# Kernel tuning notes

Measured on AMD Instinct MI355X. Metric: run time of the kernel, lower is better.

## Reference

```python
import jax, jax.numpy as jnp
import numpy as np

D_MODEL = 1024
NUM_HEADS = 16
D_K = D_MODEL // NUM_HEADS
ROPE_THETA = 10000.0


def setup_inputs() -> dict:
    key = jax.random.key(0)
    kx, kq, kk, kv, ko = jax.random.split(key, 5)
    B, S = 2, 2048
    sigma = np.sqrt(2.0) / np.sqrt(D_MODEL + D_MODEL)
    x = jax.random.normal(kx, (B, S, D_MODEL), dtype=jnp.float32)
    Wq = jax.random.normal(kq, (D_MODEL, D_MODEL), dtype=jnp.float32) * sigma
    Wk = jax.random.normal(kk, (D_MODEL, D_MODEL), dtype=jnp.float32) * sigma
    Wv = jax.random.normal(kv, (D_MODEL, D_MODEL), dtype=jnp.float32) * sigma
    Wo = jax.random.normal(ko, (D_MODEL, D_MODEL), dtype=jnp.float32) * sigma
    return {"x": x, "Wq": Wq, "Wk": Wk, "Wv": Wv, "Wo": Wo}


def _rope(t, positions):
    # t: [B, H, S, D_K], positions: [S]
    half = jnp.arange(0, D_K, 2, dtype=jnp.float32)          # [D_K/2]
    freqs = 1.0 / (ROPE_THETA ** (half / D_K))               # [D_K/2]
    angles = positions[:, None].astype(jnp.float32) * freqs  # [S, D_K/2]
    cos = jnp.cos(angles)
    sin = jnp.sin(angles)
    t_even = t[..., 0::2]
    t_odd = t[..., 1::2]
    even_rot = t_even * cos - t_odd * sin
    odd_rot = t_even * sin + t_odd * cos
    # interleave back to [..., D_K]
    return jnp.stack([even_rot, odd_rot], axis=-1).reshape(t.shape)


def reference(x, Wq, Wk, Wv, Wo):
    B, S, _ = x.shape
    # weight layout is [d_out, d_in]: y = x @ W.T
    def proj(W):
        y = jnp.einsum('bsd,ed->bse', x, W)
        return y.reshape(B, S, NUM_HEADS, D_K).transpose(0, 2, 1, 3)  # [B,H,S,Dk]
    Q, K, V = proj(Wq), proj(Wk), proj(Wv)
    positions = jnp.arange(S)
    Q = _rope(Q, positions)
    K = _rope(K, positions)
    scale = 1.0 / jnp.sqrt(jnp.asarray(D_K, dtype=x.dtype))
    scores = jnp.einsum('bhqd,bhkd->bhqk', Q, K) * scale  # [B,H,S,S]
    causal = jnp.tril(jnp.ones((S, S), dtype=bool))
    scores = jnp.where(causal, scores, -jnp.inf)
    probs = jax.nn.softmax(scores, axis=-1)
    out = jnp.einsum('bhqk,bhkd->bhqd', probs, V)          # [B,H,S,Dk]
    out = out.transpose(0, 2, 1, 3).reshape(B, S, D_MODEL)
    return jnp.einsum('bsd,ed->bse', out, Wo)
```

## Files before the change

kernel.cpp:

```cpp
#include <hip/hip_runtime.h>
#include <hip/hip_bf16.h>
#include <math.h>

#define S_LEN   2048
#define BATCH   2
#define DMODEL  1024
#define NHEADS  16
#define DKH     64
#define MROWS   (BATCH * S_LEN)

typedef __attribute__((ext_vector_type(8))) __bf16 bf16x8;
typedef __attribute__((ext_vector_type(4))) float f32x4;
typedef __attribute__((ext_vector_type(8))) unsigned short u16x8;

__device__ __forceinline__ float bfu2f(unsigned short u) {
    union { unsigned int i; float f; } v;
    v.i = ((unsigned int)u) << 16;
    return v.f;
}

__device__ __forceinline__ unsigned short f2bfu(float f) {
    union { __bf16 h; unsigned short u; } v;
    v.h = (__bf16)f;
    return v.u;
}

#define LGKM0() __builtin_amdgcn_s_waitcnt(0xc07f)

#define SROW 40

template <int QKV>
__global__ __launch_bounds__(256) void gemm_mfma(
    const void* __restrict__ Xv,
    const float* __restrict__ W0, const float* __restrict__ W1, const float* __restrict__ W2,
    unsigned short* __restrict__ Yq, unsigned short* __restrict__ Yk, unsigned short* __restrict__ Yv,
    float* __restrict__ Yf)
{
    constexpr int POOLB = QKV ? 36864 : 20480;
    __shared__ __align__(16) unsigned char pool[POOLB];

    unsigned short* As = (unsigned short*)pool;
    unsigned short* Bs = As + 128 * SROW;

    const int tid  = threadIdx.x;
    const int wave = tid >> 6;
    const int lane = tid & 63;
    const int c    = lane & 15;
    const int quad = lane >> 4;

    const int m0 = blockIdx.y * 128;
    const int n0 = blockIdx.x * 128;
    const int w_idx = QKV ? (n0 >> 10) : 0;
    const int e0    = n0 & 1023;

    const float* W = QKV ? ((w_idx == 0) ? W0 : (w_idx == 1) ? W1 : W2) : W0;

    const int mhalf = (wave & 1) * 64;
    const int nhalf = (wave >> 1) * 64;

    f32x4 acc[4][4];
#pragma unroll
    for (int i = 0; i < 4; i++)
#pragma unroll
        for (int j = 0; j < 4; j++) acc[i][j] = (f32x4){0.f, 0.f, 0.f, 0.f};

    const int lrow = tid >> 3;
    const int lkq  = tid & 7;

    for (int k0 = 0; k0 < DMODEL; k0 += 32) {
        __syncthreads();
        if (QKV) {
            const float* X = (const float*)Xv;
#pragma unroll
            for (int i = 0; i < 4; i++) {
                int row = i * 32 + lrow;
                float4 v = *(const float4*)(X + (size_t)(m0 + row) * DMODEL + k0 + lkq * 4);
                ushort4 h;
                h.x = f2bfu(v.x); h.y = f2bfu(v.y); h.z = f2bfu(v.z); h.w = f2bfu(v.w);
                *(ushort4*)(&As[row * SROW + lkq * 4]) = h;
            }
        } else {
            const unsigned short* X = (const unsigned short*)Xv;
#pragma unroll
            for (int i = 0; i < 4; i++) {
                int row = i * 32 + lrow;
                ushort4 h = *(const ushort4*)(X + (size_t)(m0 + row) * DMODEL + k0 + lkq * 4);
                *(ushort4*)(&As[row * SROW + lkq * 4]) = h;
            }
        }
#pragma unroll
        for (int i = 0; i < 4; i++) {
            int row = i * 32 + lrow;
            float4 v = *(const float4*)(W + (size_t)(e0 + row) * DMODEL + k0 + lkq * 4);
            ushort4 h;
            h.x = f2bfu(v.x); h.y = f2bfu(v.y); h.z = f2bfu(v.z); h.w = f2bfu(v.w);
            *(ushort4*)(&Bs[row * SROW + lkq * 4]) = h;
        }
        __syncthreads();

        bf16x8 af[4], bfr[4];
#pragma unroll
        for (int mt = 0; mt < 4; mt++)
            af[mt] = *(const bf16x8*)(&As[(mhalf + mt * 16 + c) * SROW + quad * 8]);
#pragma unroll
        for (int nt = 0; nt < 4; nt++)
            bfr[nt] = *(const bf16x8*)(&Bs[(nhalf + nt * 16 + c) * SROW + quad * 8]);
#pragma unroll
        for (int mt = 0; mt < 4; mt++)
#pragma unroll
            for (int nt = 0; nt < 4; nt++)
                acc[mt][nt] = __builtin_amdgcn_mfma_f32_16x16x32_bf16(af[mt], bfr[nt], acc[mt][nt], 0, 0, 0);
    }

    __syncthreads();

    if (QKV) {
        const int h = (e0 + nhalf) >> 6;
        if (w_idx < 2) {
            unsigned short* Yqk = (w_idx == 0) ? Yq : Yk;
            float* EPf = (float*)pool + wave * 16 * 68;
            const int row = lane >> 2;
            const int cg  = lane & 3;
#pragma unroll
            for (int mt = 0; mt < 4; mt++) {
                LGKM0();
#pragma unroll
                for (int nt = 0; nt < 4; nt++)
#pragma unroll
                    for (int r = 0; r < 4; r++)
                        EPf[(quad * 4 + r) * 68 + nt * 16 + c] = acc[mt][nt][r];
                LGKM0();
                float fl[16];
#pragma unroll
                for (int j = 0; j < 4; j++) {
                    float4 v = *(const float4*)(&EPf[row * 68 + cg * 16 + j * 4]);
                    fl[j * 4 + 0] = v.x; fl[j * 4 + 1] = v.y;
                    fl[j * 4 + 2] = v.z; fl[j * 4 + 3] = v.w;
                }
                int m = m0 + mhalf + mt * 16 + row;
                int s = m & (S_LEN - 1);
                int b = m >> 11;
                u16x8 o0, o1;
#pragma unroll
                for (int pi = 0; pi < 8; pi++) {
                    int p = cg * 8 + pi;
                    float freq  = exp2f(-(float)p * 0.41524101186092034f);
                    float angle = (float)s * freq;
                    float sn, cs;
                    __sincosf(angle, &sn, &cs);
                    float ev = fl[2 * pi], ov = fl[2 * pi + 1];
                    float re = ev * cs - ov * sn;
                    float ro = ev * sn + ov * cs;
                    if (pi < 4) { o0[2 * pi] = f2bfu(re); o0[2 * pi + 1] = f2bfu(ro); }
                    else        { o1[2 * (pi - 4)] = f2bfu(re); o1[2 * (pi - 4) + 1] = f2bfu(ro); }
                }
                unsigned short* dst = Yqk + (((size_t)(b * NHEADS + h)) * S_LEN + s) * DKH + cg * 16;
                *(u16x8*)(dst)     = o0;
                *(u16x8*)(dst + 8) = o1;
            }
        } else {
            unsigned short* EPb = (unsigned short*)pool + wave * 64 * 72;
            LGKM0();
#pragma unroll
            for (int nt = 0; nt < 4; nt++)
#pragma unroll
                for (int mt = 0; mt < 4; mt++)
#pragma unroll
                    for (int r = 0; r < 4; r++)
                        EPb[(nt * 16 + c) * 72 + mt * 16 + quad * 4 + r] = f2bfu(acc[mt][nt][r]);
            LGKM0();
            int mbase = m0 + mhalf;
            int s0 = mbase & (S_LEN - 1);
            int b  = mbase >> 11;
            unsigned short* dst = Yv + (((size_t)(b * NHEADS + h)) * DKH + lane) * S_LEN + s0;
#pragma unroll
            for (int j = 0; j < 8; j++)
                *(u16x8*)(dst + j * 8) = *(const u16x8*)(&EPb[lane * 72 + j * 8]);
        }
    } else {
        float* EPf = (float*)pool + wave * 16 * 68;
        const int row = lane >> 2;
        const int cg  = lane & 3;
#pragma unroll
        for (int mt = 0; mt < 4; mt++) {
            LGKM0();
#pragma unroll
            for (int nt = 0; nt < 4; nt++)
#pragma unroll
                for (int r = 0; r < 4; r++)
                    EPf[(quad * 4 + r) * 68 + nt * 16 + c] = acc[mt][nt][r];
            LGKM0();
            int m = m0 + mhalf + mt * 16 + row;
            float* dst = Yf + (size_t)m * DMODEL + n0 + nhalf + cg * 16;
#pragma unroll
            for (int j = 0; j < 4; j++)
                *(float4*)(dst + j * 4) = *(const float4*)(&EPf[row * 68 + cg * 16 + j * 4]);
        }
    }
}

__global__ __launch_bounds__(256, 4) void attn_mfma(
    const unsigned short* __restrict__ Q,
    const unsigned short* __restrict__ K,
    const unsigned short* __restrict__ Vt,
    unsigned short* __restrict__ A)
{
    __shared__ unsigned short Ks[32 * 72];
    __shared__ unsigned short Vs[64 * 40];
    __shared__ unsigned short Plds[4][16 * 40];

    const int tid  = threadIdx.x;
    const int wave = tid >> 6;
    const int lane = tid & 63;
    const int c    = lane & 15;
    const int quad = lane >> 4;

    const int bh = blockIdx.x;
    const int b  = bh >> 4;
    const int h  = bh & 15;
    const int qb = (int)(gridDim.y - 1) - (int)blockIdx.y;
    const int q0b = qb * 64;
    const int q0 = q0b + wave * 16;

    const unsigned short* Qb = Q  + (size_t)bh * S_LEN * DKH;
    const unsigned short* Kb = K  + (size_t)bh * S_LEN * DKH;
    const unsigned short* Vb = Vt + (size_t)bh * DKH * S_LEN;

    bf16x8 qf0 = *(const bf16x8*)(Qb + (q0 + c) * DKH + quad * 8);
    bf16x8 qf1 = *(const bf16x8*)(Qb + (q0 + c) * DKH + 32 + quad * 8);

    f32x4 o0 = {0.f,0.f,0.f,0.f}, o1 = o0, o2 = o0, o3 = o0;
    float l[4] = {0.f, 0.f, 0.f, 0.f};

    unsigned short* Pw = &Plds[wave][0];

    const int my_nkb   = (q0 + 16 + 31) >> 5;
    const int nkb_blk  = (q0b + 64 + 31) >> 5;
    const int kb_full  = (q0 >= 31) ? (((q0 - 31) >> 5) + 1) : 0;

    const int krow  = tid >> 3;
    const int kcol8 = (tid & 7) * 8;
    const int vrow  = tid >> 2;
    const int vcol8 = (tid & 3) * 8;

    uint4 gK = *(const uint4*)(Kb + (size_t)krow * DKH + kcol8);
    uint4 gV = *(const uint4*)(Vb + (size_t)vrow * S_LEN + vcol8);

    for (int kb = 0; kb < nkb_blk; kb++) {
        const int k0 = kb * 32;
        __syncthreads();
        *(uint4*)(&Ks[krow * 72 + kcol8]) = gK;
        *(uint4*)(&Vs[vrow * 40 + vcol8]) = gV;
        __syncthreads();
        if (kb + 1 < nkb_blk) {
            gK = *(const uint4*)(Kb + (size_t)(k0 + 32 + krow) * DKH + kcol8);
            gV = *(const uint4*)(Vb + (size_t)vrow * S_LEN + k0 + 32 + vcol8);
        }
        if (kb < my_nkb) {
            bf16x8 k00 = *(const bf16x8*)(&Ks[c * 72 + quad * 8]);
            bf16x8 k01 = *(const bf16x8*)(&Ks[c * 72 + 32 + quad * 8]);
            bf16x8 k10 = *(const bf16x8*)(&Ks[(16 + c) * 72 + quad * 8]);
            bf16x8 k11 = *(const bf16x8*)(&Ks[(16 + c) * 72 + 32 + quad * 8]);
            f32x4 s0 = {0.f,0.f,0.f,0.f}, s1 = {0.f,0.f,0.f,0.f};
            s0 = __builtin_amdgcn_mfma_f32_16x16x32_bf16(qf0, k00, s0, 0, 0, 0);
            s0 = __builtin_amdgcn_mfma_f32_16x16x32_bf16(qf1, k01, s0, 0, 0, 0);
            s1 = __builtin_amdgcn_mfma_f32_16x16x32_bf16(qf0, k10, s1, 0, 0, 0);
            s1 = __builtin_amdgcn_mfma_f32_16x16x32_bf16(qf1, k11, s1, 0, 0, 0);

            if (kb < kb_full) {
#pragma unroll
                for (int r = 0; r < 4; r++) {
                    float e0 = __expf(s0[r] * 0.125f);
                    float e1 = __expf(s1[r] * 0.125f);
                    unsigned short pb0 = f2bfu(e0);
                    unsigned short pb1 = f2bfu(e1);
                    Pw[(quad * 4 + r) * 40 + c]      = pb0;
                    Pw[(quad * 4 + r) * 40 + 16 + c] = pb1;
                    l[r] += bfu2f(pb0) + bfu2f(pb1);
                }
            } else {
#pragma unroll
                for (int r = 0; r < 4; r++) {
                    int qrow = q0 + quad * 4 + r;
                    float e0 = (k0 + c      <= qrow) ? __expf(s0[r] * 0.125f) : 0.0f;
                    float e1 = (k0 + 16 + c <= qrow) ? __expf(s1[r] * 0.125f) : 0.0f;
                    unsigned short pb0 = f2bfu(e0);
                    unsigned short pb1 = f2bfu(e1);
                    Pw[(quad * 4 + r) * 40 + c]      = pb0;
                    Pw[(quad * 4 + r) * 40 + 16 + c] = pb1;
                    l[r] += bfu2f(pb0) + bfu2f(pb1);
                }
            }
            LGKM0();

            bf16x8 pf = *(const bf16x8*)(Pw + c * 40 + quad * 8);

            bf16x8 vf0 = *(const bf16x8*)(&Vs[(0 * 16 + c) * 40 + quad * 8]);
            bf16x8 vf1 = *(const bf16x8*)(&Vs[(1 * 16 + c) * 40 + quad * 8]);
            bf16x8 vf2 = *(const bf16x8*)(&Vs[(2 * 16 + c) * 40 + quad * 8]);
            bf16x8 vf3 = *(const bf16x8*)(&Vs[(3 * 16 + c) * 40 + quad * 8]);
            o0 = __builtin_amdgcn_mfma_f32_16x16x32_bf16(pf, vf0, o0, 0, 0, 0);
            o1 = __builtin_amdgcn_mfma_f32_16x16x32_bf16(pf, vf1, o1, 0, 0, 0);
            o2 = __builtin_amdgcn_mfma_f32_16x16x32_bf16(pf, vf2, o2, 0, 0, 0);
            o3 = __builtin_amdgcn_mfma_f32_16x16x32_bf16(pf, vf3, o3, 0, 0, 0);
        }
    }

#pragma unroll
    for (int m = 1; m < 16; m <<= 1) {
#pragma unroll
        for (int r = 0; r < 4; r++) l[r] += __shfl_xor(l[r], m, 64);
    }

#pragma unroll
    for (int r = 0; r < 4; r++) {
        float inv = 1.0f / l[r];
        int s = q0 + quad * 4 + r;
        unsigned short* Ap = A + ((size_t)b * S_LEN + s) * DMODEL + h * DKH;
        Ap[0 * 16 + c] = f2bfu(o0[r] * inv);
        Ap[1 * 16 + c] = f2bfu(o1[r] * inv);
        Ap[2 * 16 + c] = f2bfu(o2[r] * inv);
        Ap[3 * 16 + c] = f2bfu(o3[r] * inv);
    }
}

extern "C" void kernel_launch(void* const* d_in, const int* in_sizes, int n_in,
                              void* d_out, int out_size, void* d_ws, size_t ws_size,
                              hipStream_t stream) {
    const float* x  = (const float*)d_in[0];
    const float* Wq = (const float*)d_in[1];
    const float* Wk = (const float*)d_in[2];
    const float* Wv = (const float*)d_in[3];
    const float* Wo = (const float*)d_in[4];
    float* out = (float*)d_out;

    unsigned short* Qw = (unsigned short*)d_ws;
    unsigned short* Kw = Qw + (size_t)MROWS * DMODEL;
    unsigned short* Vw = Kw + (size_t)MROWS * DMODEL;
    unsigned short* Aw = Vw + (size_t)MROWS * DMODEL;

    gemm_mfma<1><<<dim3(3 * DMODEL / 128, MROWS / 128), 256, 0, stream>>>(
        x, Wq, Wk, Wv, Qw, Kw, Vw, nullptr);

    attn_mfma<<<dim3(NHEADS * BATCH, S_LEN / 64), 256, 0, stream>>>(Qw, Kw, Vw, Aw);

    gemm_mfma<0><<<dim3(DMODEL / 128, MROWS / 128), 256, 0, stream>>>(
        Aw, Wo, nullptr, nullptr, nullptr, nullptr, nullptr, out);
}
```

Measured before the change: 212.6 us.

## Prefetch next K-tile into registers in GEMMs and shrink Wo GEMM M-tile

Both projection GEMMs now load the next 32-wide K slice from global memory into registers while the current tile is consumed by MFMA, so global latency overlaps with compute. The templated kernel is split into separate QKV and output-projection kernels. The output GEMM uses a 64x128 tile, doubling its grid from 256 to 512 blocks to fill more CUs. This costs extra registers per thread, which may reduce occupancy.

```diff
diff --git a/kernel.cpp b/kernel.cpp
--- a/kernel.cpp
+++ b/kernel.cpp
@@ -29,16 +29,12 @@
 
 #define SROW 40
 
-template <int QKV>
-__global__ __launch_bounds__(256) void gemm_mfma(
-    const void* __restrict__ Xv,
+__global__ __launch_bounds__(256) void gemm_qkv(
+    const float* __restrict__ X,
     const float* __restrict__ W0, const float* __restrict__ W1, const float* __restrict__ W2,
-    unsigned short* __restrict__ Yq, unsigned short* __restrict__ Yk, unsigned short* __restrict__ Yv,
-    float* __restrict__ Yf)
+    unsigned short* __restrict__ Yq, unsigned short* __restrict__ Yk, unsigned short* __restrict__ Yv)
 {
-    constexpr int POOLB = QKV ? 36864 : 20480;
-    __shared__ __align__(16) unsigned char pool[POOLB];
-
+    __shared__ __align__(16) unsigned char pool[36864];
     unsigned short* As = (unsigned short*)pool;
     unsigned short* Bs = As + 128 * SROW;
 
@@ -50,10 +46,9 @@
 
     const int m0 = blockIdx.y * 128;
     const int n0 = blockIdx.x * 128;
-    const int w_idx = QKV ? (n0 >> 10) : 0;
+    const int w_idx = n0 >> 10;
     const int e0    = n0 & 1023;
-
-    const float* W = QKV ? ((w_idx == 0) ? W0 : (w_idx == 1) ? W1 : W2) : W0;
+    const float* W = (w_idx == 0) ? W0 : (w_idx == 1) ? W1 : W2;
 
     const int mhalf = (wave & 1) * 64;
     const int nhalf = (wave >> 1) * 64;
@@ -67,36 +62,36 @@
     const int lrow = tid >> 3;
     const int lkq  = tid & 7;
 
+    float4 rA[4], rB[4];
+#pragma unroll
+    for (int i = 0; i < 4; i++) {
+        rA[i] = *(const float4*)(X + (size_t)(m0 + i * 32 + lrow) * DMODEL + lkq * 4);
+        rB[i] = *(const float4*)(W + (size_t)(e0 + i * 32 + lrow) * DMODEL + lkq * 4);
+    }
+
     for (int k0 = 0; k0 < DMODEL; k0 += 32) {
         __syncthreads();
-        if (QKV) {
-            const float* X = (const float*)Xv;
+#pragma unroll
+        for (int i = 0; i < 4; i++) {
+            ushort4 h;
+            h.x = f2bfu(rA[i].x); h.y = f2bfu(rA[i].y); h.z = f2bfu(rA[i].z); h.w = f2bfu(rA[i].w);
+            *(ushort4*)(&As[(i * 32 + lrow) * SROW + lkq * 4]) = h;
+        }
+#pragma unroll
+        for (int i = 0; i < 4; i++) {
+            ushort4 h;
+            h.x = f2bfu(rB[i].x); h.y = f2bfu(rB[i].y); h.z = f2bfu(rB[i].z); h.w = f2bfu(rB[i].w);
+            *(ushort4*)(&Bs[(i * 32 + lrow) * SROW + lkq * 4]) = h;
+        }
+        __syncthreads();
+
+        if (k0 + 32 < DMODEL) {
 #pragma unroll
             for (int i = 0; i < 4; i++) {
-                int row = i * 32 + lrow;
-                float4 v = *(const float4*)(X + (size_t)(m0 + row) * DMODEL + k0 + lkq * 4);
-                ushort4 h;
-                h.x = f2bfu(v.x); h.y = f2bfu(v.y); h.z = f2bfu(v.z); h.w = f2bfu(v.w);
-                *(ushort4*)(&As[row * SROW + lkq * 4]) = h;
+                rA[i] = *(const float4*)(X + (size_t)(m0 + i * 32 + lrow) * DMODEL + k0 + 32 + lkq * 4);
+                rB[i] = *(const float4*)(W + (size_t)(e0 + i * 32 + lrow) * DMODEL + k0 + 32 + lkq * 4);
             }
-        } else {
-            const unsigned short* X = (const unsigned short*)Xv;
-#pragma unroll
-            for (int i = 0; i < 4; i++) {
-                int row = i * 32 + lrow;
-                ushort4 h = *(const ushort4*)(X + (size_t)(m0 + row) * DMODEL + k0 + lkq * 4);
-                *(ushort4*)(&As[row * SROW + lkq * 4]) = h;
-            }
-        }
-#pragma unroll
-        for (int i = 0; i < 4; i++) {
-            int row = i * 32 + lrow;
-            float4 v = *(const float4*)(W + (size_t)(e0 + row) * DMODEL + k0 + lkq * 4);
-            ushort4 h;
-            h.x = f2bfu(v.x); h.y = f2bfu(v.y); h.z = f2bfu(v.z); h.w = f2bfu(v.w);
-            *(ushort4*)(&Bs[row * SROW + lkq * 4]) = h;
-        }
-        __syncthreads();
+        }
 
         bf16x8 af[4], bfr[4];
 #pragma unroll
@@ -114,70 +109,9 @@
 
     __syncthreads();
 
-    if (QKV) {
-        const int h = (e0 + nhalf) >> 6;
-        if (w_idx < 2) {
-            unsigned short* Yqk = (w_idx == 0) ? Yq : Yk;
-            float* EPf = (float*)pool + wave * 16 * 68;
-            const int row = lane >> 2;
-            const int cg  = lane & 3;
-#pragma unroll
-            for (int mt = 0; mt < 4; mt++) {
-                LGKM0();
-#pragma unroll
-                for (int nt = 0; nt < 4; nt++)
-#pragma unroll
-                    for (int r = 0; r < 4; r++)
-                        EPf[(quad * 4 + r) * 68 + nt * 16 + c] = acc[mt][nt][r];
-                LGKM0();
-                float fl[16];
-#pragma unroll
-                for (int j = 0; j < 4; j++) {
-                    float4 v = *(const float4*)(&EPf[row * 68 + cg * 16 + j * 4]);
-                    fl[j * 4 + 0] = v.x; fl[j * 4 + 1] = v.y;
-                    fl[j * 4 + 2] = v.z; fl[j * 4 + 3] = v.w;
-                }
-                int m = m0 + mhalf + mt * 16 + row;
-                int s = m & (S_LEN - 1);
-                int b = m >> 11;
-                u16x8 o0, o1;
-#pragma unroll
-                for (int pi = 0; pi < 8; pi++) {
-                    int p = cg * 8 + pi;
-                    float freq  = exp2f(-(float)p * 0.41524101186092034f);
-                    float angle = (float)s * freq;
-                    float sn, cs;
-                    __sincosf(angle, &sn, &cs);
-                    float ev = fl[2 * pi], ov = fl[2 * pi + 1];
-                    float re = ev * cs - ov * sn;
-                    float ro = ev * sn + ov * cs;
-                    if (pi < 4) { o0[2 * pi] = f2bfu(re); o0[2 * pi + 1] = f2bfu(ro); }
-                    else        { o1[2 * (pi - 4)] = f2bfu(re); o1[2 * (pi - 4) + 1] = f2bfu(ro); }
-                }
-                unsigned short* dst = Yqk + (((size_t)(b * NHEADS + h)) * S_LEN + s) * DKH + cg * 16;
-                *(u16x8*)(dst)     = o0;
-                *(u16x8*)(dst + 8) = o1;
-            }
-        } else {
-            unsigned short* EPb = (unsigned short*)pool + wave * 64 * 72;
-            LGKM0();
-#pragma unroll
-            for (int nt = 0; nt < 4; nt++)
-#pragma unroll
-                for (int mt = 0; mt < 4; mt++)
-#pragma unroll
-                    for (int r = 0; r < 4; r++)
-                        EPb[(nt * 16 + c) * 72 + mt * 16 + quad * 4 + r] = f2bfu(acc[mt][nt][r]);
-            LGKM0();
-            int mbase = m0 + mhalf;
-            int s0 = mbase & (S_LEN - 1);
-            int b  = mbase >> 11;
-            unsigned short* dst = Yv + (((size_t)(b * NHEADS + h)) * DKH + lane) * S_LEN + s0;
-#pragma unroll
-            for (int j = 0; j < 8; j++)
-                *(u16x8*)(dst + j * 8) = *(const u16x8*)(&EPb[lane * 72 + j * 8]);
-        }
-    } else {
+    const int h = (e0 + nhalf) >> 6;
+    if (w_idx < 2) {
+        unsigned short* Yqk = (w_idx == 0) ? Yq : Yk;
         float* EPf = (float*)pool + wave * 16 * 68;
         const int row = lane >> 2;
         const int cg  = lane & 3;
@@ -190,12 +124,149 @@
                 for (int r = 0; r < 4; r++)
                     EPf[(quad * 4 + r) * 68 + nt * 16 + c] = acc[mt][nt][r];
             LGKM0();
+            float fl[16];
+#pragma unroll
+            for (int j = 0; j < 4; j++) {
+                float4 v = *(const float4*)(&EPf[row * 68 + cg * 16 + j * 4]);
+                fl[j * 4 + 0] = v.x; fl[j * 4 + 1] = v.y;
+                fl[j * 4 + 2] = v.z; fl[j * 4 + 3] = v.w;
+            }
             int m = m0 + mhalf + mt * 16 + row;
-            float* dst = Yf + (size_t)m * DMODEL + n0 + nhalf + cg * 16;
-#pragma unroll
-            for (int j = 0; j < 4; j++)
-                *(float4*)(dst + j * 4) = *(const float4*)(&EPf[row * 68 + cg * 16 + j * 4]);
-        }
+            int s = m & (S_LEN - 1);
+            int b = m >> 11;
+            u16x8 o0, o1;
+#pragma unroll
+            for (int pi = 0; pi < 8; pi++) {
+                int p = cg * 8 + pi;
+                float freq  = exp2f(-(float)p * 0.41524101186092034f);
+                float angle = (float)s * freq;
+                float sn, cs;
+                __sincosf(angle, &sn, &cs);
+                float ev = fl[2 * pi], ov = fl[2 * pi + 1];
+                float re = ev * cs - ov * sn;
+                float ro = ev * sn + ov * cs;
+                if (pi < 4) { o0[2 * pi] = f2bfu(re); o0[2 * pi + 1] = f2bfu(ro); }
+                else        { o1[2 * (pi - 4)] = f2bfu(re); o1[2 * (pi - 4) + 1] = f2bfu(ro); }
+            }
+            unsigned short* dst = Yqk + (((size_t)(b * NHEADS + h)) * S_LEN + s) * DKH + cg * 16;
+            *(u16x8*)(dst)     = o0;
+            *(u16x8*)(dst + 8) = o1;
+        }
+    } else {
+        unsigned short* EPb = (unsigned short*)pool + wave * 64 * 72;
+        LGKM0();
+#pragma unroll
+        for (int nt = 0; nt < 4; nt++)
+#pragma unroll
+            for (int mt = 0; mt < 4; mt++)
+#pragma unroll
+                for (int r = 0; r < 4; r++)
+                    EPb[(nt * 16 + c) * 72 + mt * 16 + quad * 4 + r] = f2bfu(acc[mt][nt][r]);
+        LGKM0();
+        int mbase = m0 + mhalf;
+        int s0 = mbase & (S_LEN - 1);
+        int b  = mbase >> 11;
+        unsigned short* dst = Yv + (((size_t)(b * NHEADS + h)) * DKH + lane) * S_LEN + s0;
+#pragma unroll
+        for (int j = 0; j < 8; j++)
+            *(u16x8*)(dst + j * 8) = *(const u16x8*)(&EPb[lane * 72 + j * 8]);
+    }
+}
+
+__global__ __launch_bounds__(256) void gemm_wo(
+    const unsigned short* __restrict__ X,
+    const float* __restrict__ W,
+    float* __restrict__ Yf)
+{
+    __shared__ __align__(16) unsigned char pool[17408];
+    unsigned short* As = (unsigned short*)pool;
+    unsigned short* Bs = As + 64 * SROW;
+
+    const int tid  = threadIdx.x;
+    const int wave = tid >> 6;
+    const int lane = tid & 63;
+    const int c    = lane & 15;
+    const int quad = lane >> 4;
+
+    const int m0 = blockIdx.y * 64;
+    const int n0 = blockIdx.x * 128;
+
+    const int mhalf = (wave & 1) * 32;
+    const int nhalf = (wave >> 1) * 64;
+
+    f32x4 acc[2][4];
+#pragma unroll
+    for (int i = 0; i < 2; i++)
+#pragma unroll
+        for (int j = 0; j < 4; j++) acc[i][j] = (f32x4){0.f, 0.f, 0.f, 0.f};
+
+    const int lrow = tid >> 3;
+    const int lkq  = tid & 7;
+
+    ushort4 rA[2];
+    float4  rB[4];
+#pragma unroll
+    for (int i = 0; i < 2; i++)
+        rA[i] = *(const ushort4*)(X + (size_t)(m0 + i * 32 + lrow) * DMODEL + lkq * 4);
+#pragma unroll
+    for (int i = 0; i < 4; i++)
+        rB[i] = *(const float4*)(W + (size_t)(n0 + i * 32 + lrow) * DMODEL + lkq * 4);
+
+    for (int k0 = 0; k0 < DMODEL; k0 += 32) {
+        __syncthreads();
+#pragma unroll
+        for (int i = 0; i < 2; i++)
+            *(ushort4*)(&As[(i * 32 + lrow) * SROW + lkq * 4]) = rA[i];
+#pragma unroll
+        for (int i = 0; i < 4; i++) {
+            ushort4 h;
+            h.x = f2bfu(rB[i].x); h.y = f2bfu(rB[i].y); h.z = f2bfu(rB[i].z); h.w = f2bfu(rB[i].w);
+            *(ushort4*)(&Bs[(i * 32 + lrow) * SROW + lkq * 4]) = h;
+        }
+        __syncthreads();
+
+        if (k0 + 32 < DMODEL) {
+#pragma unroll
+            for (int i = 0; i < 2; i++)
+                rA[i] = *(const ushort4*)(X + (size_t)(m0 + i * 32 + lrow) * DMODEL + k0 + 32 + lkq * 4);
+#pragma unroll
+            for (int i = 0; i < 4; i++)
+                rB[i] = *(const float4*)(W + (size_t)(n0 + i * 32 + lrow) * DMODEL + k0 + 32 + lkq * 4);
+        }
+
+        bf16x8 af[2], bfr[4];
+#pragma unroll
+        for (int mt = 0; mt < 2; mt++)
+            af[mt] = *(const bf16x8*)(&As[(mhalf + mt * 16 + c) * SROW + quad * 8]);
+#pragma unroll
+        for (int nt = 0; nt < 4; nt++)
+            bfr[nt] = *(const bf16x8*)(&Bs[(nhalf + nt * 16 + c) * SROW + quad * 8]);
+#pragma unroll
+        for (int mt = 0; mt < 2; mt++)
+#pragma unroll
+            for (int nt = 0; nt < 4; nt++)
+                acc[mt][nt] = __builtin_amdgcn_mfma_f32_16x16x32_bf16(af[mt], bfr[nt], acc[mt][nt], 0, 0, 0);
+    }
+
+    __syncthreads();
+
+    float* EPf = (float*)pool + wave * 16 * 68;
+    const int row = lane >> 2;
+    const int cg  = lane & 3;
+#pragma unroll
+    for (int mt = 0; mt < 2; mt++) {
+        LGKM0();
+#pragma unroll
+        for (int nt = 0; nt < 4; nt++)
+#pragma unroll
+            for (int r = 0; r < 4; r++)
+                EPf[(quad * 4 + r) * 68 + nt * 16 + c] = acc[mt][nt][r];
+        LGKM0();
+        int m = m0 + mhalf + mt * 16 + row;
+        float* dst = Yf + (size_t)m * DMODEL + n0 + nhalf + cg * 16;
+#pragma unroll
+        for (int j = 0; j < 4; j++)
+            *(float4*)(dst + j * 4) = *(const float4*)(&EPf[row * 68 + cg * 16 + j * 4]);
     }
 }
 
@@ -339,11 +410,10 @@
     unsigned short* Vw = Kw + (size_t)MROWS * DMODEL;
     unsigned short* Aw = Vw + (size_t)MROWS * DMODEL;
 
-    gemm_mfma<1><<<dim3(3 * DMODEL / 128, MROWS / 128), 256, 0, stream>>>(
-        x, Wq, Wk, Wv, Qw, Kw, Vw, nullptr);
+    gemm_qkv<<<dim3(3 * DMODEL / 128, MROWS / 128), 256, 0, stream>>>(
+        x, Wq, Wk, Wv, Qw, Kw, Vw);
 
     attn_mfma<<<dim3(NHEADS * BATCH, S_LEN / 64), 256, 0, stream>>>(Qw, Kw, Vw, Aw);
 
-    gemm_mfma<0><<<dim3(DMODEL / 128, MROWS / 128), 256, 0, stream>>>(
-        Aw, Wo, nullptr, nullptr, nullptr, nullptr, nullptr, out);
-}
+    gemm_wo<<<dim3(DMODEL / 128, MROWS / 64), 256, 0, stream>>>(Aw, Wo, out);
+}
```

Measured after the change: 202.1 us. -4.9%, faster.
